# Kernel tuning notes

Measured on AMD Instinct MI355X. Metric: run time of the kernel, lower is better.

## Reference

```python
import jax, jax.numpy as jnp
import numpy as np

TOP_K = 2


def setup_inputs() -> dict:
    key = jax.random.key(0)
    k1, k2, k3, k4 = jax.random.split(key, 4)
    B, S, D, F, E = 4, 2048, 1024, 4096, 8
    return {
        "inputs": jax.random.normal(k1, (B, S, D), dtype=jnp.float32),
        "gate_w": jax.random.normal(k2, (D, E), dtype=jnp.float32) * 0.02,
        "w1": jax.random.normal(k3, (E, D, F), dtype=jnp.float32) * 0.02,
        "w2": jax.random.normal(k4, (E, F, D), dtype=jnp.float32) * 0.02,
    }


def reference(inputs, gate_w, w1, w2):
    # gate logits: [B, S, E]
    gate_logits = jnp.einsum("bsd,de->bse", inputs, gate_w)
    E = gate_logits.shape[-1]

    # router KL loss (matches F.kl_div(log(mean_prob), uniform, reduction='batchmean')):
    # kl = sum(u * (log u - log p_mean)) / E   (batchmean divides by first dim = E)
    gate_prob = jax.nn.softmax(gate_logits.astype(jnp.float32), axis=-1).astype(inputs.dtype)
    mean_prob = gate_prob.mean(axis=(0, 1))  # [E]
    u = jnp.full((E,), 1.0 / E, dtype=mean_prob.dtype)
    kl_loss = jnp.sum(u * (jnp.log(u) - jnp.log(mean_prob))) / E

    # top-k routing
    weights, selected = jax.lax.top_k(gate_logits, TOP_K)  # [B,S,k]
    prob = jax.nn.softmax(weights.astype(jnp.float32), axis=-1).astype(inputs.dtype)

    # combine weight per expert: [B,S,E]; zero for unselected experts
    onehot = jax.nn.one_hot(selected, E, dtype=prob.dtype)  # [B,S,k,E]
    combine = jnp.einsum("bsk,bske->bse", prob, onehot)

    results = jnp.zeros_like(inputs)
    for i in range(E):  # fixed small loop over experts
        h = jax.nn.silu(jnp.einsum("bsd,df->bsf", inputs, w1[i]))
        out = jnp.einsum("bsf,fd->bsd", h, w2[i])
        results = results + combine[..., i : i + 1] * out
    return (results, kl_loss)
```

## Files before the change

kernel.cpp:

```cpp
#include <hip/hip_runtime.h>
#include <hip/hip_bf16.h>
#include <cstdint>


#define N_TOK 8192
#define D_DIM 1024
#define F_DIM 4096
#define N_EXP 8
#define MB_MAX 72

#define CNT_OFF   0u
#define HOFF_OFF  64u
#define NMB_OFF   104u
#define ZPG_OFF   128u
#define MBE_OFF   256u
#define MBB_OFF   896u
#define PSUM_OFF  1536u
#define LIST_OFF  67072u
#define COEF_OFF  329216u
#define H1_OFF    1048576ull
#define XBF_OFF   1048576ull
#define W1T_OFF   18874368ull
#define W2T_OFF   (W1T_OFF + 67108864ull)
#define H2_OFF    (W2T_OFF + 67108864ull)
#define FULL_WS   (H2_OFF + 18432ull * 4096ull * 2ull)

typedef __attribute__((ext_vector_type(8))) short short8;
typedef __attribute__((ext_vector_type(4))) float f32x4;
typedef __attribute__((ext_vector_type(4))) float float4v;
typedef __attribute__((ext_vector_type(2))) unsigned int u32x2;

__device__ __forceinline__ unsigned short f2bf(float x) {
  unsigned int u = __float_as_uint(x);
  unsigned int r = (u + 0x7fffu + ((u >> 16) & 1u)) >> 16;
  return (unsigned short)r;
}

__device__ __forceinline__ void gload16(const void* g, void* l) {
  __builtin_amdgcn_global_load_lds(
      (const __attribute__((address_space(1))) void*)g,
      (__attribute__((address_space(3))) void*)l, 16, 0, 0);
}

__global__ void router_kernel(const float* __restrict__ x,
                              const float* __restrict__ gw,
                              int* __restrict__ cnt, int* __restrict__ list,
                              float* __restrict__ coef,
                              float* __restrict__ psum,
                              unsigned short* __restrict__ xbf) {
  const int wave = threadIdx.x >> 6;
  const int lane = threadIdx.x & 63;
  const int t = blockIdx.x * 4 + wave;

  __shared__ float bps[N_EXP];
  if (threadIdx.x < N_EXP) bps[threadIdx.x] = 0.f;
  __syncthreads();

  float lg[8] = {0.f, 0.f, 0.f, 0.f, 0.f, 0.f, 0.f, 0.f};
  const float* xr = x + (size_t)t * D_DIM;
  unsigned short* xbr = xbf + (size_t)t * D_DIM;
#pragma unroll
  for (int i = 0; i < 16; ++i) {
    int d = lane + i * 64;
    float xv = xr[d];
    xbr[d] = f2bf(xv);
    float4v w0 = *(const float4v*)(gw + d * 8);
    float4v w1 = *(const float4v*)(gw + d * 8 + 4);
    lg[0] = fmaf(xv, w0.x, lg[0]); lg[1] = fmaf(xv, w0.y, lg[1]);
    lg[2] = fmaf(xv, w0.z, lg[2]); lg[3] = fmaf(xv, w0.w, lg[3]);
    lg[4] = fmaf(xv, w1.x, lg[4]); lg[5] = fmaf(xv, w1.y, lg[5]);
    lg[6] = fmaf(xv, w1.z, lg[6]); lg[7] = fmaf(xv, w1.w, lg[7]);
  }
#pragma unroll
  for (int m = 32; m; m >>= 1) {
#pragma unroll
    for (int e = 0; e < 8; ++e) lg[e] += __shfl_xor(lg[e], m);
  }

  if (lane == 0) {
    float mx = lg[0];
#pragma unroll
    for (int e = 1; e < 8; ++e) mx = fmaxf(mx, lg[e]);
    float p[8], s = 0.f;
#pragma unroll
    for (int e = 0; e < 8; ++e) { p[e] = expf(lg[e] - mx); s += p[e]; }
    float inv = 1.f / s;
#pragma unroll
    for (int e = 0; e < 8; ++e) atomicAdd(&bps[e], p[e] * inv);

    int i0 = 0;
#pragma unroll
    for (int e = 1; e < 8; ++e) if (lg[e] > lg[i0]) i0 = e;
    int i1 = (i0 == 0) ? 1 : 0;
#pragma unroll
    for (int e = 0; e < 8; ++e) if (e != i1 && e != i0 && lg[e] > lg[i1]) i1 = e;
    float p0 = 1.f / (1.f + expf(lg[i1] - lg[i0]));
    float p1 = 1.f - p0;
    int s0 = atomicAdd(&cnt[i0], 1);
    list[i0 * N_TOK + s0] = t; coef[i0 * N_TOK + s0] = p0;
    int s1 = atomicAdd(&cnt[i1], 1);
    list[i1 * N_TOK + s1] = t; coef[i1 * N_TOK + s1] = p1;
  }
  __syncthreads();
  if (threadIdx.x < 8) psum[blockIdx.x * 8 + threadIdx.x] = bps[threadIdx.x];
}

__global__ void prefix_kernel(const int* __restrict__ cnt, int* __restrict__ hoff,
                              int* __restrict__ mbe, int* __restrict__ mbb,
                              int* __restrict__ nmb, int g) {
  if (threadIdx.x == 0) {
    int o = 0, gmb = 0;
    for (int e = 0; e < 8; ++e) {
      hoff[e] = o;
      int nb = (cnt[e] + g - 1) / g;
      for (int m = 0; m < nb; ++m) { mbe[gmb] = e; mbb[gmb] = m; ++gmb; }
      o += nb * g;
    }
    hoff[8] = o;
    *nmb = gmb;
  }
}

__global__ void kl_kernel(const float* __restrict__ psum, float* __restrict__ out_kl) {
  __shared__ float s[8];
  if (threadIdx.x < 8) s[threadIdx.x] = 0.f;
  __syncthreads();
  float loc[8] = {0.f, 0.f, 0.f, 0.f, 0.f, 0.f, 0.f, 0.f};
  for (int r = threadIdx.x; r < 2048; r += 256) {
#pragma unroll
    for (int e = 0; e < 8; ++e) loc[e] += psum[r * 8 + e];
  }
#pragma unroll
  for (int e = 0; e < 8; ++e) atomicAdd(&s[e], loc[e]);
  __syncthreads();
  if (threadIdx.x == 0) {
    float kl = 0.f;
#pragma unroll
    for (int e = 0; e < 8; ++e) {
      float mean = s[e] / 8192.f;
      kl += (logf(0.125f) - logf(mean));
    }
    out_kl[0] = kl * (0.125f * 0.125f);
  }
}

__global__ __launch_bounds__(256) void wtrans_kernel(
    const float* __restrict__ w, unsigned short* __restrict__ wt, int K, int N) {
  const int e = blockIdx.z;
  const int n0 = blockIdx.x * 64, k0 = blockIdx.y * 64;
  __shared__ float t[64][65];
  const float* we = w + (size_t)e * K * N;
  const int nl = threadIdx.x & 63;
  const int kl4 = threadIdx.x >> 6;
#pragma unroll
  for (int r = 0; r < 16; ++r) {
    int kl = r * 4 + kl4;
    t[kl][nl] = we[(size_t)(k0 + kl) * N + n0 + nl];
  }
  __syncthreads();
  unsigned short* wte = wt + (size_t)e * K * N;
  const int kp = (threadIdx.x & 31) * 2;
  const int nl8 = threadIdx.x >> 5;
#pragma unroll
  for (int r = 0; r < 8; ++r) {
    int n = r * 8 + nl8;
    unsigned int pk = (unsigned int)f2bf(t[kp][n]) |
                      ((unsigned int)f2bf(t[kp + 1][n]) << 16);
    *(unsigned int*)(wte + (size_t)(n0 + n) * K + k0 + kp) = pk;
  }
}

__device__ __forceinline__ short8 ld_frag(const unsigned short* base, int row_base,
                                          int k_base, int lane) {
  int row = row_base + (lane & 15);
  int byte = (row * 128 + (k_base + ((lane >> 4) << 3)) * 2) ^ ((row & 7) << 4);
  return *(const short8*)((const char*)base + byte);
}

#define STAGE(dst_bo)                                                      \
  {                                                                        \
    char* la_ = (char*)As + (dst_bo) + tid * 16;                           \
    char* lb_ = (char*)Bs + (dst_bo) + tid * 16;                           \
    _Pragma("unroll") for (int i_ = 0; i_ < 4; ++i_) {                     \
      gload16(asrc[i_], la_ + i_ * 8192);                                  \
      gload16(bsrc[i_], lb_ + i_ * 8192);                                  \
      asrc[i_] += astep[i_];                                               \
      bsrc[i_] += 128;                                                     \
    }                                                                      \
  }

#define COMPUTE(bo)                                                        \
  {                                                                        \
    const unsigned short* At_ = (const unsigned short*)((const char*)As + (bo)); \
    const unsigned short* Bt_ = (const unsigned short*)((const char*)Bs + (bo)); \
    _Pragma("unroll") for (int ks_ = 0; ks_ < 2; ++ks_) {                  \
      short8 bb[4];                                                        \
      _Pragma("unroll") for (int nf_ = 0; nf_ < 4; ++nf_)                  \
        bb[nf_] = ld_frag(Bt_, wn + nf_ * 16, ks_ * 32, lane);             \
      _Pragma("unroll") for (int mh_ = 0; mh_ < 2; ++mh_) {                \
        short8 af[4];                                                      \
        _Pragma("unroll") for (int m4_ = 0; m4_ < 4; ++m4_)                \
          af[m4_] = ld_frag(At_, wm + mh_ * 64 + m4_ * 16, ks_ * 32, lane);\
        __builtin_amdgcn_s_setprio(1);                                     \
        _Pragma("unroll") for (int m4_ = 0; m4_ < 4; ++m4_)                \
          _Pragma("unroll") for (int nf_ = 0; nf_ < 4; ++nf_)              \
            acc[mh_ * 4 + m4_][nf_] = __builtin_amdgcn_mfma_f32_16x16x32_bf16( \
                af[m4_], bb[nf_], acc[mh_ * 4 + m4_][nf_], 0, 0, 0);       \
        __builtin_amdgcn_s_setprio(0);                                     \
      }                                                                    \
    }                                                                      \
  }

#define KLOOP2(NT)                                                         \
  {                                                                        \
    STAGE(0);                                                              \
    __syncthreads();                                                       \
    int bo = 0;                                                            \
    for (int t_ = 0; t_ < (NT) - 1; ++t_) {                                \
      STAGE(bo ^ 32768);                                                   \
      COMPUTE(bo);                                                         \
      __syncthreads();                                                     \
      bo ^= 32768;                                                         \
    }                                                                      \
    COMPUTE(bo);                                                           \
  }

__global__ __launch_bounds__(512, 2) void gemm1_v8(
    const unsigned short* __restrict__ xbf, const unsigned short* __restrict__ w1t,
    const int* __restrict__ cnt, const int* __restrict__ hoff,
    const int* __restrict__ mbe, const int* __restrict__ mbb,
    const int* __restrict__ nmb,
    const int* __restrict__ list, const unsigned short* __restrict__ zpage,
    unsigned short* __restrict__ h) {
  const int mb = blockIdx.x;
  if (mb >= *nmb) return;
  const int e = mbe[mb], mblk = mbb[mb], nblk = blockIdx.y;
  const int c = cnt[e];
  const int tid = threadIdx.x, lane = tid & 63, wave = tid >> 6;
  const int wm = (wave >> 2) * 128, wn = (wave & 3) * 64;

  __shared__ unsigned short As[2][16384];
  __shared__ unsigned short Bs[2][16384];

  const int rowb = tid >> 3;
  const int sw = (((tid & 7) ^ (rowb & 7)) << 4);
  const char* asrc[4]; int astep[4];
  const char* bsrc[4];
#pragma unroll
  for (int i = 0; i < 4; ++i) {
    int row = i * 64 + rowb;
    int slot = mblk * 256 + row;
    if (slot < c) {
      int tok = list[e * N_TOK + slot];
      asrc[i] = (const char*)(xbf + (size_t)tok * D_DIM) + sw;
      astep[i] = 128;
    } else {
      asrc[i] = (const char*)zpage + sw;
      astep[i] = 0;
    }
    bsrc[i] = (const char*)(w1t + ((size_t)e * F_DIM + nblk * 256 + i * 64 + rowb) * D_DIM) + sw;
  }

  f32x4 acc[8][4];
#pragma unroll
  for (int i = 0; i < 8; ++i)
#pragma unroll
    for (int j = 0; j < 4; ++j) acc[i][j] = f32x4{0.f, 0.f, 0.f, 0.f};

  KLOOP2(16);

  const int hbase = hoff[e] + mblk * 256;
#pragma unroll
  for (int mf = 0; mf < 8; ++mf)
#pragma unroll
    for (int nf = 0; nf < 4; ++nf)
#pragma unroll
      for (int r = 0; r < 4; ++r) {
        float v = acc[mf][nf][r];
        v = v / (1.f + __expf(-v));
        int row = wm + mf * 16 + ((lane >> 4) << 2) + r;
        int col = nblk * 256 + wn + nf * 16 + (lane & 15);
        h[(size_t)(hbase + row) * F_DIM + col] = f2bf(v);
      }
}

__global__ __launch_bounds__(512, 2) void gemm2_v8(
    const unsigned short* __restrict__ h, const unsigned short* __restrict__ w2t,
    const int* __restrict__ cnt, const int* __restrict__ hoff,
    const int* __restrict__ mbe, const int* __restrict__ mbb,
    const int* __restrict__ nmb,
    const int* __restrict__ list, const float* __restrict__ coef,
    float* __restrict__ out) {
  const int mb = blockIdx.x;
  if (mb >= *nmb) return;
  const int e = mbe[mb], mblk = mbb[mb];
  const int nblk = blockIdx.y & 3;
  const int kofs = (blockIdx.y >> 2) * 2048;
  const int c = cnt[e];
  const int tid = threadIdx.x, lane = tid & 63, wave = tid >> 6;
  const int wm = (wave >> 2) * 128, wn = (wave & 3) * 64;

  __shared__ unsigned short As[2][16384];
  __shared__ unsigned short Bs[2][16384];

  const int rowb = tid >> 3;
  const int sw = (((tid & 7) ^ (rowb & 7)) << 4);
  const int hbase = hoff[e] + mblk * 256;
  const char* asrc[4]; int astep[4];
  const char* bsrc[4];
#pragma unroll
  for (int i = 0; i < 4; ++i) {
    asrc[i] = (const char*)(h + (size_t)(hbase + i * 64 + rowb) * F_DIM + kofs) + sw;
    astep[i] = 128;
    bsrc[i] = (const char*)(w2t + ((size_t)e * D_DIM + nblk * 256 + i * 64 + rowb) * F_DIM + kofs) + sw;
  }

  f32x4 acc[8][4];
#pragma unroll
  for (int i = 0; i < 8; ++i)
#pragma unroll
    for (int j = 0; j < 4; ++j) acc[i][j] = f32x4{0.f, 0.f, 0.f, 0.f};

  KLOOP2(32);

#pragma unroll
  for (int mf = 0; mf < 8; ++mf) {
#pragma unroll
    for (int r = 0; r < 4; ++r) {
      int slot = mblk * 256 + wm + mf * 16 + ((lane >> 4) << 2) + r;
      if (slot < c) {
        int tok = list[e * N_TOK + slot];
        float cf = coef[e * N_TOK + slot];
#pragma unroll
        for (int nf = 0; nf < 4; ++nf) {
          int col = nblk * 256 + wn + nf * 16 + (lane & 15);
          unsafeAtomicAdd(&out[(size_t)tok * D_DIM + col], cf * acc[mf][nf][r]);
        }
      }
    }
  }
}

__global__ __launch_bounds__(256) void gemm1_v1(
    const float* __restrict__ x, const float* __restrict__ w1,
    const int* __restrict__ cnt, const int* __restrict__ hoff,
    const int* __restrict__ list, unsigned short* __restrict__ h) {
  const int e = blockIdx.z, mblk = blockIdx.y, nblk = blockIdx.x;
  const int c = cnt[e];
  if (mblk * 128 >= c) return;
  const int tid = threadIdx.x, lane = tid & 63, wave = tid >> 6;
  const int wm = (wave >> 1) * 64, wn = (wave & 1) * 64;

  __shared__ unsigned short At[128 * 64];
  __shared__ unsigned short Bt[128 * 64];
  __shared__ int toks[128];
  if (tid < 128) {
    int slot = mblk * 128 + tid;
    toks[tid] = (slot < c) ? list[e * N_TOK + slot] : -1;
  }
  __syncthreads();

  f32x4 acc[4][4];
#pragma unroll
  for (int i = 0; i < 4; ++i)
#pragma unroll
    for (int j = 0; j < 4; ++j) acc[i][j] = f32x4{0.f, 0.f, 0.f, 0.f};

  const float* w1e = w1 + (size_t)e * D_DIM * F_DIM;
  for (int kc = 0; kc < 16; ++kc) {
    __syncthreads();
#pragma unroll
    for (int it = 0; it < 8; ++it) {
      int lin = it * 256 + tid;
      int row = lin >> 4, c4 = lin & 15;
      int tok = toks[row];
      unsigned int lo = 0u, hi = 0u;
      if (tok >= 0) {
        float4v f = *(const float4v*)(x + (size_t)tok * D_DIM + kc * 64 + c4 * 4);
        lo = (unsigned int)f2bf(f.x) | ((unsigned int)f2bf(f.y) << 16);
        hi = (unsigned int)f2bf(f.z) | ((unsigned int)f2bf(f.w) << 16);
      }
      int byte = (row * 128 + c4 * 8) ^ ((row & 7) << 4);
      *(u32x2*)((char*)At + byte) = u32x2{lo, hi};
    }
#pragma unroll
    for (int it = 0; it < 16; ++it) {
      int lin = it * 256 + tid;
      int f_loc = lin & 127, dp = lin >> 7;
      int d = kc * 64 + dp * 2;
      const float* src = w1e + (size_t)d * F_DIM + nblk * 128 + f_loc;
      unsigned int pk = (unsigned int)f2bf(src[0]) |
                        ((unsigned int)f2bf(src[F_DIM]) << 16);
      int byte = (f_loc * 128 + dp * 4) ^ ((f_loc & 7) << 4);
      *(unsigned int*)((char*)Bt + byte) = pk;
    }
    __syncthreads();
#pragma unroll
    for (int ks = 0; ks < 2; ++ks) {
      short8 af[4], bb[4];
#pragma unroll
      for (int mf = 0; mf < 4; ++mf) af[mf] = ld_frag(At, wm + mf * 16, ks * 32, lane);
#pragma unroll
      for (int nf = 0; nf < 4; ++nf) bb[nf] = ld_frag(Bt, wn + nf * 16, ks * 32, lane);
#pragma unroll
      for (int mf = 0; mf < 4; ++mf)
#pragma unroll
        for (int nf = 0; nf < 4; ++nf)
          acc[mf][nf] = __builtin_amdgcn_mfma_f32_16x16x32_bf16(
              af[mf], bb[nf], acc[mf][nf], 0, 0, 0);
    }
  }

  const int hbase = hoff[e] + mblk * 128;
#pragma unroll
  for (int mf = 0; mf < 4; ++mf)
#pragma unroll
    for (int nf = 0; nf < 4; ++nf)
#pragma unroll
      for (int r = 0; r < 4; ++r) {
        float v = acc[mf][nf][r];
        v = v / (1.f + __expf(-v));
        int row = wm + mf * 16 + ((lane >> 4) << 2) + r;
        int col = nblk * 128 + wn + nf * 16 + (lane & 15);
        h[(size_t)(hbase + row) * F_DIM + col] = f2bf(v);
      }
}

__global__ __launch_bounds__(256) void gemm2_v1(
    const unsigned short* __restrict__ h, const float* __restrict__ w2,
    const int* __restrict__ cnt, const int* __restrict__ hoff,
    const int* __restrict__ list, const float* __restrict__ coef,
    float* __restrict__ out) {
  const int e = blockIdx.z, mblk = blockIdx.y, nblk = blockIdx.x;
  const int c = cnt[e];
  if (mblk * 128 >= c) return;
  const int tid = threadIdx.x, lane = tid & 63, wave = tid >> 6;
  const int wm = (wave >> 1) * 64, wn = (wave & 1) * 64;

  __shared__ unsigned short At[128 * 64];
  __shared__ unsigned short Bt[128 * 64];

  f32x4 acc[4][4];
#pragma unroll
  for (int i = 0; i < 4; ++i)
#pragma unroll
    for (int j = 0; j < 4; ++j) acc[i][j] = f32x4{0.f, 0.f, 0.f, 0.f};

  const int hbase = hoff[e] + mblk * 128;
  const float* w2e = w2 + (size_t)e * F_DIM * D_DIM;
  for (int kc = 0; kc < 64; ++kc) {
    __syncthreads();
#pragma unroll
    for (int it = 0; it < 8; ++it) {
      int lin = it * 256 + tid;
      int row = lin >> 4, c4 = lin & 15;
      u32x2 v = *(const u32x2*)(h + (size_t)(hbase + row) * F_DIM + kc * 64 + c4 * 4);
      int byte = (row * 128 + c4 * 8) ^ ((row & 7) << 4);
      *(u32x2*)((char*)At + byte) = v;
    }
#pragma unroll
    for (int it = 0; it < 16; ++it) {
      int lin = it * 256 + tid;
      int dcol = lin & 127, kp = lin >> 7;
      int k = kc * 64 + kp * 2;
      const float* src = w2e + (size_t)k * D_DIM + nblk * 128 + dcol;
      unsigned int pk = (unsigned int)f2bf(src[0]) |
                        ((unsigned int)f2bf(src[D_DIM]) << 16);
      int byte = (dcol * 128 + kp * 4) ^ ((dcol & 7) << 4);
      *(unsigned int*)((char*)Bt + byte) = pk;
    }
    __syncthreads();
#pragma unroll
    for (int ks = 0; ks < 2; ++ks) {
      short8 af[4], bb[4];
#pragma unroll
      for (int mf = 0; mf < 4; ++mf) af[mf] = ld_frag(At, wm + mf * 16, ks * 32, lane);
#pragma unroll
      for (int nf = 0; nf < 4; ++nf) bb[nf] = ld_frag(Bt, wn + nf * 16, ks * 32, lane);
#pragma unroll
      for (int mf = 0; mf < 4; ++mf)
#pragma unroll
        for (int nf = 0; nf < 4; ++nf)
          acc[mf][nf] = __builtin_amdgcn_mfma_f32_16x16x32_bf16(
              af[mf], bb[nf], acc[mf][nf], 0, 0, 0);
    }
  }

#pragma unroll
  for (int mf = 0; mf < 4; ++mf) {
#pragma unroll
    for (int r = 0; r < 4; ++r) {
      int slot = mblk * 128 + wm + mf * 16 + ((lane >> 4) << 2) + r;
      if (slot < c) {
        int tok = list[e * N_TOK + slot];
        float cf = coef[e * N_TOK + slot];
#pragma unroll
        for (int nf = 0; nf < 4; ++nf) {
          int col = nblk * 128 + wn + nf * 16 + (lane & 15);
          unsafeAtomicAdd(&out[(size_t)tok * D_DIM + col], cf * acc[mf][nf][r]);
        }
      }
    }
  }
}

extern "C" void kernel_launch(void* const* d_in, const int* in_sizes, int n_in,
                              void* d_out, int out_size, void* d_ws, size_t ws_size,
                              hipStream_t stream) {
  const float* x = (const float*)d_in[0];
  const float* gw = (const float*)d_in[1];
  const float* w1 = (const float*)d_in[2];
  const float* w2 = (const float*)d_in[3];
  float* out = (float*)d_out;
  char* ws = (char*)d_ws;

  int* cnt = (int*)(ws + CNT_OFF);
  int* hoff = (int*)(ws + HOFF_OFF);
  int* nmb = (int*)(ws + NMB_OFF);
  int* mbe = (int*)(ws + MBE_OFF);
  int* mbb = (int*)(ws + MBB_OFF);
  float* psum = (float*)(ws + PSUM_OFF);
  int* list = (int*)(ws + LIST_OFF);
  float* coef = (float*)(ws + COEF_OFF);
  unsigned short* xbf = (unsigned short*)(ws + XBF_OFF);

  const bool full = (ws_size >= FULL_WS);

  hipMemsetAsync(d_ws, 0, PSUM_OFF + 2048 * 8 * 4, stream);
  hipMemsetAsync(d_out, 0, (size_t)out_size * 4, stream);

  router_kernel<<<2048, 256, 0, stream>>>(x, gw, cnt, list, coef, psum, xbf);
  prefix_kernel<<<1, 64, 0, stream>>>(cnt, hoff, mbe, mbb, nmb, full ? 256 : 128);
  kl_kernel<<<1, 256, 0, stream>>>(psum, out + 8388608);

  if (full) {
    unsigned short* w1t = (unsigned short*)(ws + W1T_OFF);
    unsigned short* w2t = (unsigned short*)(ws + W2T_OFF);
    unsigned short* h = (unsigned short*)(ws + H2_OFF);
    const unsigned short* zpage = (const unsigned short*)(ws + ZPG_OFF);

    wtrans_kernel<<<dim3(64, 16, 8), 256, 0, stream>>>(w1, w1t, 1024, 4096);
    wtrans_kernel<<<dim3(16, 64, 8), 256, 0, stream>>>(w2, w2t, 4096, 1024);
    gemm1_v8<<<dim3(MB_MAX, 16), 512, 0, stream>>>(xbf, w1t, cnt, hoff, mbe, mbb,
                                                   nmb, list, zpage, h);
    gemm2_v8<<<dim3(MB_MAX, 8), 512, 0, stream>>>(h, w2t, cnt, hoff, mbe, mbb,
                                                  nmb, list, coef, out);
  } else {
    unsigned short* h = (unsigned short*)(ws + H1_OFF);
    gemm1_v1<<<dim3(32, 64, 8), 256, 0, stream>>>(x, w1, cnt, hoff, list, h);
    gemm2_v1<<<dim3(8, 64, 8), 256, 0, stream>>>(h, w2, cnt, hoff, list, coef, out);
  }
}
```

Measured before the change: 849.0 us.

## Load A fragments directly from global memory, shrink tiles to 256x128

The A operand (tokens or hidden activations) now skips LDS staging. Each wave reads its MFMA fragments straight from global memory through per-row pointers, and only the weight tile is double-buffered in shared memory. Blocks drop to 256 threads with a 256x128 output tile, and the grid grows to match. The aim is to cut LDS traffic and shared memory use so occupancy can rise, but uncoalesced per-lane 16-byte global loads for A, with no prefetch, may expose memory latency and re-read A across more N-blocks.

```diff
diff --git a/kernel.cpp b/kernel.cpp
--- a/kernel.cpp
+++ b/kernel.cpp
@@ -12,7 +12,6 @@
 #define CNT_OFF   0u
 #define HOFF_OFF  64u
 #define NMB_OFF   104u
-#define ZPG_OFF   128u
 #define MBE_OFF   256u
 #define MBB_OFF   896u
 #define PSUM_OFF  1536u
@@ -177,21 +176,17 @@
   return *(const short8*)((const char*)base + byte);
 }
 
-#define STAGE(dst_bo)                                                      \
+#define STAGE_B(dst_bo)                                                    \
   {                                                                        \
-    char* la_ = (char*)As + (dst_bo) + tid * 16;                           \
     char* lb_ = (char*)Bs + (dst_bo) + tid * 16;                           \
     _Pragma("unroll") for (int i_ = 0; i_ < 4; ++i_) {                     \
-      gload16(asrc[i_], la_ + i_ * 8192);                                  \
-      gload16(bsrc[i_], lb_ + i_ * 8192);                                  \
-      asrc[i_] += astep[i_];                                               \
+      gload16(bsrc[i_], lb_ + i_ * 4096);                                  \
       bsrc[i_] += 128;                                                     \
     }                                                                      \
   }
 
-#define COMPUTE(bo)                                                        \
+#define COMPUTE9(bo)                                                       \
   {                                                                        \
-    const unsigned short* At_ = (const unsigned short*)((const char*)As + (bo)); \
     const unsigned short* Bt_ = (const unsigned short*)((const char*)Bs + (bo)); \
     _Pragma("unroll") for (int ks_ = 0; ks_ < 2; ++ks_) {                  \
       short8 bb[4];                                                        \
@@ -200,7 +195,7 @@
       _Pragma("unroll") for (int mh_ = 0; mh_ < 2; ++mh_) {                \
         short8 af[4];                                                      \
         _Pragma("unroll") for (int m4_ = 0; m4_ < 4; ++m4_)                \
-          af[m4_] = ld_frag(At_, wm + mh_ * 64 + m4_ * 16, ks_ * 32, lane);\
+          af[m4_] = *(const short8*)(aptr[mh_ * 4 + m4_] + ks_ * 32);      \
         __builtin_amdgcn_s_setprio(1);                                     \
         _Pragma("unroll") for (int m4_ = 0; m4_ < 4; ++m4_)                \
           _Pragma("unroll") for (int nf_ = 0; nf_ < 4; ++nf_)              \
@@ -209,56 +204,51 @@
         __builtin_amdgcn_s_setprio(0);                                     \
       }                                                                    \
     }                                                                      \
-  }
-
-#define KLOOP2(NT)                                                         \
+    _Pragma("unroll") for (int mf_ = 0; mf_ < 8; ++mf_) aptr[mf_] += 64;   \
+  }
+
+#define KLOOP9(NT)                                                         \
   {                                                                        \
-    STAGE(0);                                                              \
+    STAGE_B(0);                                                            \
     __syncthreads();                                                       \
     int bo = 0;                                                            \
     for (int t_ = 0; t_ < (NT) - 1; ++t_) {                                \
-      STAGE(bo ^ 32768);                                                   \
-      COMPUTE(bo);                                                         \
+      STAGE_B(bo ^ 16384);                                                 \
+      COMPUTE9(bo);                                                        \
       __syncthreads();                                                     \
-      bo ^= 32768;                                                         \
+      bo ^= 16384;                                                         \
     }                                                                      \
-    COMPUTE(bo);                                                           \
-  }
-
-__global__ __launch_bounds__(512, 2) void gemm1_v8(
+    COMPUTE9(bo);                                                          \
+  }
+
+__global__ __launch_bounds__(256, 2) void gemm1_v9(
     const unsigned short* __restrict__ xbf, const unsigned short* __restrict__ w1t,
     const int* __restrict__ cnt, const int* __restrict__ hoff,
     const int* __restrict__ mbe, const int* __restrict__ mbb,
     const int* __restrict__ nmb,
-    const int* __restrict__ list, const unsigned short* __restrict__ zpage,
-    unsigned short* __restrict__ h) {
+    const int* __restrict__ list, unsigned short* __restrict__ h) {
   const int mb = blockIdx.x;
   if (mb >= *nmb) return;
   const int e = mbe[mb], mblk = mbb[mb], nblk = blockIdx.y;
   const int c = cnt[e];
   const int tid = threadIdx.x, lane = tid & 63, wave = tid >> 6;
-  const int wm = (wave >> 2) * 128, wn = (wave & 3) * 64;
-
-  __shared__ unsigned short As[2][16384];
-  __shared__ unsigned short Bs[2][16384];
+  const int wm = (wave >> 1) * 128, wn = (wave & 1) * 64;
+
+  __shared__ unsigned short Bs[2][8192];
 
   const int rowb = tid >> 3;
   const int sw = (((tid & 7) ^ (rowb & 7)) << 4);
-  const char* asrc[4]; int astep[4];
   const char* bsrc[4];
 #pragma unroll
-  for (int i = 0; i < 4; ++i) {
-    int row = i * 64 + rowb;
-    int slot = mblk * 256 + row;
-    if (slot < c) {
-      int tok = list[e * N_TOK + slot];
-      asrc[i] = (const char*)(xbf + (size_t)tok * D_DIM) + sw;
-      astep[i] = 128;
-    } else {
-      asrc[i] = (const char*)zpage + sw;
-      astep[i] = 0;
-    }
-    bsrc[i] = (const char*)(w1t + ((size_t)e * F_DIM + nblk * 256 + i * 64 + rowb) * D_DIM) + sw;
+  for (int i = 0; i < 4; ++i)
+    bsrc[i] = (const char*)(w1t + ((size_t)e * F_DIM + nblk * 128 + i * 32 + rowb) * D_DIM) + sw;
+
+  const unsigned short* aptr[8];
+#pragma unroll
+  for (int mf = 0; mf < 8; ++mf) {
+    int slot = mblk * 256 + wm + mf * 16 + (lane & 15);
+    int tok = (slot < c) ? list[e * N_TOK + slot] : 0;
+    aptr[mf] = xbf + (size_t)tok * D_DIM + ((lane >> 4) << 3);
   }
 
   f32x4 acc[8][4];
@@ -267,7 +257,7 @@
 #pragma unroll
     for (int j = 0; j < 4; ++j) acc[i][j] = f32x4{0.f, 0.f, 0.f, 0.f};
 
-  KLOOP2(16);
+  KLOOP9(16);
 
   const int hbase = hoff[e] + mblk * 256;
 #pragma unroll
@@ -279,12 +269,12 @@
         float v = acc[mf][nf][r];
         v = v / (1.f + __expf(-v));
         int row = wm + mf * 16 + ((lane >> 4) << 2) + r;
-        int col = nblk * 256 + wn + nf * 16 + (lane & 15);
+        int col = nblk * 128 + wn + nf * 16 + (lane & 15);
         h[(size_t)(hbase + row) * F_DIM + col] = f2bf(v);
       }
 }
 
-__global__ __launch_bounds__(512, 2) void gemm2_v8(
+__global__ __launch_bounds__(256, 2) void gemm2_v9(
     const unsigned short* __restrict__ h, const unsigned short* __restrict__ w2t,
     const int* __restrict__ cnt, const int* __restrict__ hoff,
     const int* __restrict__ mbe, const int* __restrict__ mbb,
@@ -294,25 +284,27 @@
   const int mb = blockIdx.x;
   if (mb >= *nmb) return;
   const int e = mbe[mb], mblk = mbb[mb];
-  const int nblk = blockIdx.y & 3;
-  const int kofs = (blockIdx.y >> 2) * 2048;
+  const int nblk = blockIdx.y & 7;
+  const int kofs = (blockIdx.y >> 3) * 2048;
   const int c = cnt[e];
   const int tid = threadIdx.x, lane = tid & 63, wave = tid >> 6;
-  const int wm = (wave >> 2) * 128, wn = (wave & 3) * 64;
-
-  __shared__ unsigned short As[2][16384];
-  __shared__ unsigned short Bs[2][16384];
+  const int wm = (wave >> 1) * 128, wn = (wave & 1) * 64;
+
+  __shared__ unsigned short Bs[2][8192];
 
   const int rowb = tid >> 3;
   const int sw = (((tid & 7) ^ (rowb & 7)) << 4);
+  const char* bsrc[4];
+#pragma unroll
+  for (int i = 0; i < 4; ++i)
+    bsrc[i] = (const char*)(w2t + ((size_t)e * D_DIM + nblk * 128 + i * 32 + rowb) * F_DIM + kofs) + sw;
+
   const int hbase = hoff[e] + mblk * 256;
-  const char* asrc[4]; int astep[4];
-  const char* bsrc[4];
-#pragma unroll
-  for (int i = 0; i < 4; ++i) {
-    asrc[i] = (const char*)(h + (size_t)(hbase + i * 64 + rowb) * F_DIM + kofs) + sw;
-    astep[i] = 128;
-    bsrc[i] = (const char*)(w2t + ((size_t)e * D_DIM + nblk * 256 + i * 64 + rowb) * F_DIM + kofs) + sw;
+  const unsigned short* aptr[8];
+#pragma unroll
+  for (int mf = 0; mf < 8; ++mf) {
+    int row = wm + mf * 16 + (lane & 15);
+    aptr[mf] = h + (size_t)(hbase + row) * F_DIM + kofs + ((lane >> 4) << 3);
   }
 
   f32x4 acc[8][4];
@@ -321,7 +313,7 @@
 #pragma unroll
     for (int j = 0; j < 4; ++j) acc[i][j] = f32x4{0.f, 0.f, 0.f, 0.f};
 
-  KLOOP2(32);
+  KLOOP9(32);
 
 #pragma unroll
   for (int mf = 0; mf < 8; ++mf) {
@@ -333,7 +325,7 @@
         float cf = coef[e * N_TOK + slot];
 #pragma unroll
         for (int nf = 0; nf < 4; ++nf) {
-          int col = nblk * 256 + wn + nf * 16 + (lane & 15);
+          int col = nblk * 128 + wn + nf * 16 + (lane & 15);
           unsafeAtomicAdd(&out[(size_t)tok * D_DIM + col], cf * acc[mf][nf][r]);
         }
       }
@@ -537,14 +529,13 @@
     unsigned short* w1t = (unsigned short*)(ws + W1T_OFF);
     unsigned short* w2t = (unsigned short*)(ws + W2T_OFF);
     unsigned short* h = (unsigned short*)(ws + H2_OFF);
-    const unsigned short* zpage = (const unsigned short*)(ws + ZPG_OFF);
 
     wtrans_kernel<<<dim3(64, 16, 8), 256, 0, stream>>>(w1, w1t, 1024, 4096);
     wtrans_kernel<<<dim3(16, 64, 8), 256, 0, stream>>>(w2, w2t, 4096, 1024);
-    gemm1_v8<<<dim3(MB_MAX, 16), 512, 0, stream>>>(xbf, w1t, cnt, hoff, mbe, mbb,
-                                                   nmb, list, zpage, h);
-    gemm2_v8<<<dim3(MB_MAX, 8), 512, 0, stream>>>(h, w2t, cnt, hoff, mbe, mbb,
-                                                  nmb, list, coef, out);
+    gemm1_v9<<<dim3(MB_MAX, 32), 256, 0, stream>>>(xbf, w1t, cnt, hoff, mbe, mbb,
+                                                   nmb, list, h);
+    gemm2_v9<<<dim3(MB_MAX, 16), 256, 0, stream>>>(h, w2t, cnt, hoff, mbe, mbb,
+                                                   nmb, list, coef, out);
   } else {
     unsigned short* h = (unsigned short*)(ws + H1_OFF);
     gemm1_v1<<<dim3(32, 64, 8), 256, 0, stream>>>(x, w1, cnt, hoff, list, h);
```

After: 1.117 ms, median of 2. 31.5% more time.
